# Kernel optimization log

Measured on AMD Instinct MI355X. Metric: run time of the kernel, lower is better.

The kernel has to match this reference:

```python
import jax, jax.numpy as jnp
import numpy as np

NEG = -1e30  # log-space 'minus infinity' that stays finite in fp32 arithmetic
BLANK = 0


def _lse3(a, b, c):
    m = jnp.maximum(jnp.maximum(a, b), c)
    return m + jnp.log(jnp.exp(a - m) + jnp.exp(b - m) + jnp.exp(c - m))


def setup_inputs() -> dict:
    key = jax.random.key(0)
    k1, k2, k3, k4 = jax.random.split(key, 4)
    B, T, C, L = 16, 512, 4096, 128
    scores = jax.random.normal(k1, (B, T, C), dtype=jnp.float32)
    labels = jax.random.randint(k2, (B, L), 1, C, dtype=jnp.int64)      # no blanks in targets
    feat_lens = jax.random.randint(k3, (B,), 384, T + 1, dtype=jnp.int64)
    label_lens = jax.random.randint(k4, (B,), 64, L + 1, dtype=jnp.int64)
    return {"scores": scores, "labels": labels, "feat_lens": feat_lens, "label_lens": label_lens}


def reference(scores, labels, feat_lens, label_lens):
    # scores: [B, T, C]. Matches torch: log_softmax then nn.CTCLoss(blank=0,
    # reduction='mean', zero_infinity=True).
    scores = scores.astype(jnp.float32)
    log_probs = jax.nn.log_softmax(scores, axis=-1)                      # [B, T, C]
    B, T, C = scores.shape
    L = labels.shape[1]
    S = 2 * L + 1  # extended label: blank, l1, blank, ..., lL, blank

    ext = jnp.full((B, S), BLANK, dtype=labels.dtype).at[:, 1::2].set(labels)
    # Gather per-(t, extended-symbol) log-probs once: [B, T, S]
    lp = jnp.take_along_axis(log_probs, jnp.broadcast_to(ext[:, None, :], (B, T, S)), axis=2)

    # skip transition s-2 -> s allowed iff ext[s] != blank and ext[s] != ext[s-2]
    skip = jnp.concatenate(
        [jnp.zeros((B, 2), bool), (ext[:, 2:] != ext[:, :-2]) & (ext[:, 2:] != BLANK)], axis=1)

    alpha0 = jnp.full((B, S), NEG, dtype=jnp.float32).at[:, 0].set(lp[:, 0, 0])
    alpha0 = alpha0.at[:, 1].set(jnp.where(label_lens > 0, lp[:, 0, 1], NEG))

    lp_t_first = jnp.swapaxes(lp, 0, 1)  # [T, B, S]

    def step(alpha, xs):
        lp_t, t = xs
        a1 = jnp.pad(alpha, ((0, 0), (1, 0)), constant_values=NEG)[:, :S]
        a2 = jnp.pad(alpha, ((0, 0), (2, 0)), constant_values=NEG)[:, :S]
        a2 = jnp.where(skip, a2, NEG)
        new = lp_t + _lse3(alpha, a1, a2)
        alpha = jnp.where((t < feat_lens)[:, None], new, alpha)  # freeze past feat_len
        return alpha, None

    alpha, _ = jax.lax.scan(step, alpha0, (lp_t_first[1:], jnp.arange(1, T)))

    end = 2 * label_lens  # index of final blank per sample
    a_end = jnp.take_along_axis(alpha, end[:, None], axis=1)[:, 0]
    a_end1 = jnp.where(
        label_lens > 0,
        jnp.take_along_axis(alpha, jnp.maximum(end - 1, 0)[:, None], axis=1)[:, 0], NEG)
    m = jnp.maximum(a_end, a_end1)
    log_lik = m + jnp.log(jnp.exp(a_end - m) + jnp.exp(a_end1 - m))
    loss = -log_lik
    loss = jnp.where(loss > 0.5e30, 0.0, loss)  # zero_infinity=True
    denom = jnp.maximum(label_lens, 1).astype(loss.dtype)
    return jnp.mean(loss / denom)  # torch 'mean': divide by target_lengths, then batch mean
```

## Files before the change

kernel.cpp:

```cpp
#include <hip/hip_runtime.h>

#define T_ 512
#define C_ 4096
#define L_ 128
#define RCPLN2 1.4426950408889634f
#define LN2 0.6931471805599453f
#define NEGL (-1e30f)
#define SCALE_CTR 4.722366482869645e21f
#define SCALE_LOG 72.0f

__device__ __forceinline__ float fexp2(float x) { return __builtin_amdgcn_exp2f(x); }
__device__ __forceinline__ float flog2(float x) { return __builtin_amdgcn_logf(x); }
__device__ __forceinline__ float frcp(float x)  { return __builtin_amdgcn_rcpf(x); }
__device__ __forceinline__ float lg(float x)    { return (x > 0.f) ? flog2(x) : NEGL; }

template <int CTRL>
__device__ __forceinline__ float dppmov(float v) {
  return __int_as_float(__builtin_amdgcn_update_dpp(
      0, __float_as_int(v), CTRL, 0xF, 0xF, true));
}
__device__ __forceinline__ float wshr1(float v) { return dppmov<0x138>(v); }
__device__ __forceinline__ float wshl1(float v) { return dppmov<0x130>(v); }
template <int CTRL>
__device__ __forceinline__ float maxdpp(float v) {
  return fmaxf(v, dppmov<CTRL>(v));
}
__device__ __forceinline__ float wavemax(float v) {
  v = maxdpp<0xB1>(v);
  v = maxdpp<0x4E>(v);
  v = maxdpp<0x141>(v);
  v = maxdpp<0x140>(v);
  v = maxdpp<0x142>(v);
  v = maxdpp<0x143>(v);
  return __int_as_float(__builtin_amdgcn_readlane(__float_as_int(v), 63));
}

__global__ __launch_bounds__(256) void k_lse_gather(
    const float* __restrict__ scores, const int* __restrict__ labels,
    const int* __restrict__ feat_lens,
    float* __restrict__ p_lab, float* __restrict__ p_blank,
    int* __restrict__ dpDone, float* __restrict__ lossAcc) {
  const int row = blockIdx.x;
  const int b = row >> 9;
  const int t = row & (T_ - 1);
  if (row == 0 && threadIdx.x == 0) {
    atomicExch(dpDone, 0);
    atomicExch(lossAcc, 0.0f);
  }
  if (t >= feat_lens[b]) return;

  __shared__ float sRow[C_];
  __shared__ float sSum[4];
  const float4* __restrict__ rp4 = (const float4*)(scores + (size_t)row * C_);
  float4* sRow4 = (float4*)sRow;
  const int tid = threadIdx.x;

  float s0 = 0.f, s1 = 0.f, s2 = 0.f, s3 = 0.f;
#pragma unroll
  for (int k = 0; k < 4; ++k) {
    float4 v = rp4[tid + 256 * k];
    sRow4[tid + 256 * k] = v;
    s0 += fexp2(v.x * RCPLN2);
    s1 += fexp2(v.y * RCPLN2);
    s2 += fexp2(v.z * RCPLN2);
    s3 += fexp2(v.w * RCPLN2);
  }
  float s = (s0 + s1) + (s2 + s3);
#pragma unroll
  for (int off = 32; off; off >>= 1) s += __shfl_down(s, off);
  const int wid = tid >> 6, lane = tid & 63;
  if (lane == 0) sSum[wid] = s;
  __syncthreads();
  const float l2sum = flog2((sSum[0] + sSum[1]) + (sSum[2] + sSum[3]));

  if (tid < L_) {
    const int lab = labels[b * L_ + tid];
    p_lab[(size_t)row * L_ + tid] = fexp2(sRow[lab] * RCPLN2 - l2sum);
  } else if (tid == L_) {
    p_blank[row] = fexp2(sRow[0] * RCPLN2 - l2sum);
  }
}

__global__ __launch_bounds__(128) void k_ctc_dp(
    const float* __restrict__ p_lab, const float* __restrict__ p_blank,
    const int* __restrict__ labels, const int* __restrict__ feat_lens,
    const int* __restrict__ label_lens, int* __restrict__ dpDone,
    float* __restrict__ lossAcc, float* __restrict__ out, int B) {
  const int b = blockIdx.x;
  const int lane = threadIdx.x & 63;
  const int wid = threadIdx.x >> 6;
  const int flen = feat_lens[b];
  const int llen = label_lens[b];
  const int tm = (flen >> 1) & ~3;

  const int l0 = labels[b * L_ + 2 * lane];
  const int l1 = labels[b * L_ + 2 * lane + 1];
  const int lm1 = __shfl_up(l1, 1);
  const int ln0 = __shfl_down(l0, 1);
  const bool skip1 = (lane > 0) && (l0 != lm1);
  const bool skip3 = (l1 != l0);
  const bool skipd = (lane < 63) && (ln0 != l1);

  const float2* __restrict__ llp = (const float2*)(p_lab + (size_t)b * T_ * L_);
  const float* __restrict__ lpl = p_lab + (size_t)b * T_ * L_;
  const float* __restrict__ lbp = p_blank + b * T_;

  __shared__ float sB[257];
  __shared__ float sSb;

  if (wid == 0) {
    const float2 ll0 = llp[lane];
    float a0 = (lane == 0) ? lbp[0] : 0.f;
    float a1 = (lane == 0) ? ll0.x : 0.f;
    float a2 = 0.f, a3 = 0.f, a4 = 0.f;
    float p = 0.f;
    float Sa = 0.f;

    float2 cc[4], nc[4], mc[4]; float cb[4], nb[4], mb[4];
#pragma unroll
    for (int k = 0; k < 4; ++k) {
      cc[k] = llp[(1 + k) * 64 + lane]; cb[k] = lbp[1 + k];
    }
#pragma unroll
    for (int k = 0; k < 4; ++k) {
      const int tt = min(5 + k, flen - 1);
      nc[k] = llp[tt * 64 + lane]; nb[k] = lbp[tt];
    }
#pragma unroll
    for (int k = 0; k < 4; ++k) {
      const int tt = min(9 + k, flen - 1);
      mc[k] = llp[tt * 64 + lane]; mb[k] = lbp[tt];
    }
    int t = 1;
    while (t <= tm) {
      float2 oc[4]; float ob[4];
#pragma unroll
      for (int k = 0; k < 4; ++k) {
        const int tt = min(t + 12 + k, flen - 1);
        oc[k] = llp[tt * 64 + lane]; ob[k] = lbp[tt];
      }
#pragma unroll
      for (int k = 0; k < 4; ++k) {
        const float n3 = cc[k].y * (a3 + a2 + (skip3 ? a1 : 0.f));
        const float n4 = cb[k] * (a4 + a3);
        const float pn = wshr1(n3);
        const float n0 = cb[k] * (a0 + p);
        const float n1 = cc[k].x * (a1 + a0 + (skip1 ? p : 0.f));
        const float n2 = cb[k] * (a2 + a1);
        a0 = n0; a1 = n1; a2 = n2; a3 = n3;
        a4 = (lane == 63) ? n4 : 0.f;
        p = pn;
        if (k & 1) {
          float m = wavemax(fmaxf(fmaxf(fmaxf(a0, a1), fmaxf(a2, a3)), a4));
          m = fmaxf(m, 1e-35f);
          const float r = frcp(m) * SCALE_CTR;
          Sa += flog2(m) - SCALE_LOG;
          a0 *= r; a1 *= r; a2 *= r; a3 *= r; a4 *= r; p *= r;
        }
      }
#pragma unroll
      for (int k = 0; k < 4; ++k) { cc[k] = nc[k]; cb[k] = nb[k];
                                    nc[k] = mc[k]; nb[k] = mb[k];
                                    mc[k] = oc[k]; mb[k] = ob[k]; }
      t += 4;
    }
    const float2 cce = llp[tm * 64 + lane];
    const float cbe = lbp[tm];
    const float lb2 = flog2(cbe), lc0 = flog2(cce.x), lc1 = flog2(cce.y);
    const float la0 = lg(a0), la1 = lg(a1), la2 = lg(a2), la3 = lg(a3);
    const float la4 = lg(a4);
    __syncthreads();
    float w0 = la0 + sB[4 * lane + 0] - lb2;
    float w1 = la1 + sB[4 * lane + 1] - lc0;
    float w2 = la2 + sB[4 * lane + 2] - lb2;
    float w3 = la3 + sB[4 * lane + 3] - lc1;
    float m = fmaxf(fmaxf(w0, w1), fmaxf(w2, w3));
    float w4 = NEGL;
    if (lane == 63) { w4 = la4 + sB[256] - lb2; m = fmaxf(m, w4); }
#pragma unroll
    for (int off = 1; off < 64; off <<= 1) m = fmaxf(m, __shfl_xor(m, off));
    float sum = fexp2(w0 - m) + fexp2(w1 - m) + fexp2(w2 - m) + fexp2(w3 - m);
    if (lane == 63) sum += fexp2(w4 - m);
#pragma unroll
    for (int off = 1; off < 64; off <<= 1) sum += __shfl_xor(sum, off);
    if (lane == 0) {
      const float l2lik = m + flog2(sum) + Sa + sSb;
      float loss = -LN2 * l2lik;
      if (!(fabsf(loss) < 0.5e30f)) loss = 0.0f;
      atomicAdd(lossAcc, loss / (float)llen);
      const int done = __hip_atomic_fetch_add(dpDone, 1, __ATOMIC_ACQ_REL,
                                              __HIP_MEMORY_SCOPE_AGENT);
      if (done == B - 1)
        out[0] = atomicAdd(lossAcc, 0.0f) / (float)B;
    }
  } else {
    const int e = 2 * llen;
    const float ve = lbp[flen - 1];
    const float vo = lpl[(size_t)(flen - 1) * L_ + (llen - 1)];
    float b0 = (4 * lane == e) ? ve : 0.f;
    float b1 = (4 * lane + 1 == e - 1) ? vo : 0.f;
    float b2 = (4 * lane + 2 == e) ? ve : 0.f;
    float b3 = (4 * lane + 3 == e - 1) ? vo : 0.f;
    float b4 = (lane == 63 && e == 256) ? ve : 0.f;
    float q0 = __shfl_down(b0, 1); q0 = (lane == 63) ? b4 : q0;
    float q1 = __shfl_down(b1, 1); q1 = (lane == 63) ? 0.f : q1;
    float Sb = 0.f;

    float2 cc[4], nc[4], mc[4]; float cb[4], nb[4], mb[4];
    int t = flen - 2;
#pragma unroll
    for (int k = 0; k < 4; ++k) {
      const int tt = max(t - k, tm);
      cc[k] = llp[tt * 64 + lane]; cb[k] = lbp[tt];
    }
#pragma unroll
    for (int k = 0; k < 4; ++k) {
      const int tt = max(t - 4 - k, tm);
      nc[k] = llp[tt * 64 + lane]; nb[k] = lbp[tt];
    }
#pragma unroll
    for (int k = 0; k < 4; ++k) {
      const int tt = max(t - 8 - k, tm);
      mc[k] = llp[tt * 64 + lane]; mb[k] = lbp[tt];
    }
    while (t >= tm) {
      float2 oc[4]; float ob[4];
#pragma unroll
      for (int k = 0; k < 4; ++k) {
        const int tt = max(t - 12 - k, tm);
        oc[k] = llp[tt * 64 + lane]; ob[k] = lbp[tt];
      }
#pragma unroll
      for (int k = 0; k < 4; ++k) {
        if (t - k >= tm) {
          const float n0 = cb[k] * (b0 + b1);
          const float n1 = cc[k].x * (b1 + b2 + (skip3 ? b3 : 0.f));
          const float n4 = cb[k] * b4;
          const float q0n = wshl1(n0);
          const float q1n = wshl1(n1);
          const float n3 = cc[k].y * (b3 + q0 + (skipd ? q1 : 0.f));
          const float n2 = cb[k] * (b2 + b3);
          b0 = n0; b1 = n1; b2 = n2; b3 = n3; b4 = n4;
          q0 = (lane == 63) ? n4 : q0n;
          q1 = q1n;
        }
        if (k & 1) {
          float m = wavemax(fmaxf(fmaxf(fmaxf(b0, b1), fmaxf(b2, b3)), b4));
          m = fmaxf(m, 1e-35f);
          const float r = frcp(m) * SCALE_CTR;
          Sb += flog2(m) - SCALE_LOG;
          b0 *= r; b1 *= r; b2 *= r; b3 *= r; b4 *= r; q0 *= r; q1 *= r;
        }
      }
#pragma unroll
      for (int k = 0; k < 4; ++k) { cc[k] = nc[k]; cb[k] = nb[k];
                                    nc[k] = mc[k]; nb[k] = mb[k];
                                    mc[k] = oc[k]; mb[k] = ob[k]; }
      t -= 4;
    }
    sB[4 * lane + 0] = lg(b0);
    sB[4 * lane + 1] = lg(b1);
    sB[4 * lane + 2] = lg(b2);
    sB[4 * lane + 3] = lg(b3);
    if (lane == 63) sB[256] = lg(b4);
    if (lane == 0) sSb = Sb;
    __syncthreads();
  }
}

extern "C" void kernel_launch(void* const* d_in, const int* in_sizes, int n_in,
                              void* d_out, int out_size, void* d_ws, size_t ws_size,
                              hipStream_t stream) {
  const float* scores = (const float*)d_in[0];
  const int* labels = (const int*)d_in[1];
  const int* feat_lens = (const int*)d_in[2];
  const int* label_lens = (const int*)d_in[3];
  const int B = in_sizes[2];

  int* dpDone = (int*)d_ws;
  float* lossAcc = (float*)d_ws + 1;
  float* p_lab = (float*)d_ws + 64;
  float* p_blank = p_lab + (size_t)B * T_ * L_;
  float* out = (float*)d_out;

  k_lse_gather<<<B * T_, 256, 0, stream>>>(scores, labels, feat_lens,
                                           p_lab, p_blank, dpDone, lossAcc);
  k_ctc_dp<<<B, 128, 0, stream>>>(p_lab, p_blank, labels, feat_lens, label_lens,
                                  dpDone, lossAcc, out, B);
}
```

Before: 221.7 us.

## Stage forward/backward CTC probabilities through shared memory in 32-step chunks

Replaces the per-wave register prefetch pipeline of global loads with a cooperative staging scheme. Each 32-timestep chunk of label and blank probabilities for both the forward and backward passes is loaded into shared memory by all 128 threads using float4 loads, followed by a barrier. Each wave then runs its recurrence reading from LDS. This takes global-load latency off the serial DP chain, but adds two block barriers per chunk and couples the forward and backward waves, so neither can run ahead of the other.

```diff
diff --git a/kernel.cpp b/kernel.cpp
--- a/kernel.cpp
+++ b/kernel.cpp
@@ -87,8 +87,9 @@
     const int* __restrict__ label_lens, int* __restrict__ dpDone,
     float* __restrict__ lossAcc, float* __restrict__ out, int B) {
   const int b = blockIdx.x;
-  const int lane = threadIdx.x & 63;
-  const int wid = threadIdx.x >> 6;
+  const int tid = threadIdx.x;
+  const int lane = tid & 63;
+  const int wid = tid >> 6;
   const int flen = feat_lens[b];
   const int llen = label_lens[b];
   const int tm = (flen >> 1) & ~3;
@@ -105,65 +106,126 @@
   const float* __restrict__ lpl = p_lab + (size_t)b * T_ * L_;
   const float* __restrict__ lbp = p_blank + b * T_;
 
+  __shared__ float sF[32][132];
+  __shared__ float sG[32][132];
   __shared__ float sB[257];
   __shared__ float sSb;
 
+  float a0 = 0.f, a1 = 0.f, a2 = 0.f, a3 = 0.f, a4 = 0.f, pp = 0.f, Sa = 0.f;
+  float b0 = 0.f, b1 = 0.f, b2 = 0.f, b3 = 0.f, b4 = 0.f, q0 = 0.f, q1 = 0.f,
+        Sb = 0.f;
   if (wid == 0) {
     const float2 ll0 = llp[lane];
-    float a0 = (lane == 0) ? lbp[0] : 0.f;
-    float a1 = (lane == 0) ? ll0.x : 0.f;
-    float a2 = 0.f, a3 = 0.f, a4 = 0.f;
-    float p = 0.f;
-    float Sa = 0.f;
-
-    float2 cc[4], nc[4], mc[4]; float cb[4], nb[4], mb[4];
-#pragma unroll
-    for (int k = 0; k < 4; ++k) {
-      cc[k] = llp[(1 + k) * 64 + lane]; cb[k] = lbp[1 + k];
+    a0 = (lane == 0) ? lbp[0] : 0.f;
+    a1 = (lane == 0) ? ll0.x : 0.f;
+  } else {
+    const int e = 2 * llen;
+    const float ve = lbp[flen - 1];
+    const float vo = lpl[(size_t)(flen - 1) * L_ + (llen - 1)];
+    b0 = (4 * lane == e) ? ve : 0.f;
+    b1 = (4 * lane + 1 == e - 1) ? vo : 0.f;
+    b2 = (4 * lane + 2 == e) ? ve : 0.f;
+    b3 = (4 * lane + 3 == e - 1) ? vo : 0.f;
+    b4 = (lane == 63 && e == 256) ? ve : 0.f;
+    q0 = __shfl_down(b0, 1); q0 = (lane == 63) ? b4 : q0;
+    q1 = __shfl_down(b1, 1); q1 = (lane == 63) ? 0.f : q1;
+  }
+
+  int tf = 1;
+  int tb = flen - 2;
+  const int nb = flen - 1 - tm;
+  const int NS = ((tm > nb ? tm : nb) + 31) >> 5;
+
+  for (int ss = 0; ss < NS; ++ss) {
+    const int t0f = 1 + (ss << 5);
+    const int t0b = flen - 2 - (ss << 5);
+    {
+      const int rg = tid >> 5;
+      const int c4 = (tid & 31) << 2;
+#pragma unroll
+      for (int r8 = 0; r8 < 8; ++r8) {
+        const int r = (r8 << 2) + rg;
+        const int tF = min(t0f + r, T_ - 1);
+        const int tB = max(t0b - r, 0);
+        const float4 v = *(const float4*)(lpl + (size_t)tF * L_ + c4);
+        const float4 w = *(const float4*)(lpl + (size_t)tB * L_ + c4);
+        *(float4*)&sF[r][c4] = v;
+        *(float4*)&sG[r][c4] = w;
+      }
+      if (tid >= 64) {
+        const int i = tid - 64;
+        if (i < 32) sF[i][128] = lbp[min(t0f + i, T_ - 1)];
+        else        sG[i - 32][128] = lbp[max(t0b - (i - 32), 0)];
+      }
     }
-#pragma unroll
-    for (int k = 0; k < 4; ++k) {
-      const int tt = min(5 + k, flen - 1);
-      nc[k] = llp[tt * 64 + lane]; nb[k] = lbp[tt];
+    __syncthreads();
+    if (wid == 0) {
+      for (int c = 0; c < 8; ++c) {
+        if (tf <= tm) {
+          const int rbase = tf - t0f;
+#pragma unroll
+          for (int k = 0; k < 4; ++k) {
+            const int r = rbase + k;
+            const float2 cck = *(const float2*)&sF[r][2 * lane];
+            const float cbk = sF[r][128];
+            const float n3 = cck.y * (a3 + a2 + (skip3 ? a1 : 0.f));
+            const float n4 = cbk * (a4 + a3);
+            const float pn = wshr1(n3);
+            const float n0 = cbk * (a0 + pp);
+            const float n1 = cck.x * (a1 + a0 + (skip1 ? pp : 0.f));
+            const float n2 = cbk * (a2 + a1);
+            a0 = n0; a1 = n1; a2 = n2; a3 = n3;
+            a4 = (lane == 63) ? n4 : 0.f;
+            pp = pn;
+            if (k & 1) {
+              float m = wavemax(fmaxf(fmaxf(fmaxf(a0, a1), fmaxf(a2, a3)), a4));
+              m = fmaxf(m, 1e-35f);
+              const float r2 = frcp(m) * SCALE_CTR;
+              Sa += flog2(m) - SCALE_LOG;
+              a0 *= r2; a1 *= r2; a2 *= r2; a3 *= r2; a4 *= r2; pp *= r2;
+            }
+          }
+          tf += 4;
+        }
+      }
+    } else {
+      for (int c = 0; c < 8; ++c) {
+        if (tb >= tm) {
+          const int rbase = t0b - tb;
+#pragma unroll
+          for (int k = 0; k < 4; ++k) {
+            if (tb - k >= tm) {
+              const int r = rbase + k;
+              const float2 cck = *(const float2*)&sG[r][2 * lane];
+              const float cbk = sG[r][128];
+              const float n0 = cbk * (b0 + b1);
+              const float n1 = cck.x * (b1 + b2 + (skip3 ? b3 : 0.f));
+              const float n4 = cbk * b4;
+              const float q0n = wshl1(n0);
+              const float q1n = wshl1(n1);
+              const float n3 = cck.y * (b3 + q0 + (skipd ? q1 : 0.f));
+              const float n2 = cbk * (b2 + b3);
+              b0 = n0; b1 = n1; b2 = n2; b3 = n3; b4 = n4;
+              q0 = (lane == 63) ? n4 : q0n;
+              q1 = q1n;
+            }
+            if (k & 1) {
+              float m = wavemax(fmaxf(fmaxf(fmaxf(b0, b1), fmaxf(b2, b3)), b4));
+              m = fmaxf(m, 1e-35f);
+              const float r2 = frcp(m) * SCALE_CTR;
+              Sb += flog2(m) - SCALE_LOG;
+              b0 *= r2; b1 *= r2; b2 *= r2; b3 *= r2; b4 *= r2;
+              q0 *= r2; q1 *= r2;
+            }
+          }
+          tb -= 4;
+        }
+      }
     }
-#pragma unroll
-    for (int k = 0; k < 4; ++k) {
-      const int tt = min(9 + k, flen - 1);
-      mc[k] = llp[tt * 64 + lane]; mb[k] = lbp[tt];
-    }
-    int t = 1;
-    while (t <= tm) {
-      float2 oc[4]; float ob[4];
-#pragma unroll
-      for (int k = 0; k < 4; ++k) {
-        const int tt = min(t + 12 + k, flen - 1);
-        oc[k] = llp[tt * 64 + lane]; ob[k] = lbp[tt];
-      }
-#pragma unroll
-      for (int k = 0; k < 4; ++k) {
-        const float n3 = cc[k].y * (a3 + a2 + (skip3 ? a1 : 0.f));
-        const float n4 = cb[k] * (a4 + a3);
-        const float pn = wshr1(n3);
-        const float n0 = cb[k] * (a0 + p);
-        const float n1 = cc[k].x * (a1 + a0 + (skip1 ? p : 0.f));
-        const float n2 = cb[k] * (a2 + a1);
-        a0 = n0; a1 = n1; a2 = n2; a3 = n3;
-        a4 = (lane == 63) ? n4 : 0.f;
-        p = pn;
-        if (k & 1) {
-          float m = wavemax(fmaxf(fmaxf(fmaxf(a0, a1), fmaxf(a2, a3)), a4));
-          m = fmaxf(m, 1e-35f);
-          const float r = frcp(m) * SCALE_CTR;
-          Sa += flog2(m) - SCALE_LOG;
-          a0 *= r; a1 *= r; a2 *= r; a3 *= r; a4 *= r; p *= r;
-        }
-      }
-#pragma unroll
-      for (int k = 0; k < 4; ++k) { cc[k] = nc[k]; cb[k] = nb[k];
-                                    nc[k] = mc[k]; nb[k] = mb[k];
-                                    mc[k] = oc[k]; mb[k] = ob[k]; }
-      t += 4;
-    }
+    __syncthreads();
+  }
+
+  if (wid == 0) {
     const float2 cce = llp[tm * 64 + lane];
     const float cbe = lbp[tm];
     const float lb2 = flog2(cbe), lc0 = flog2(cce.x), lc1 = flog2(cce.y);
@@ -194,70 +256,6 @@
         out[0] = atomicAdd(lossAcc, 0.0f) / (float)B;
     }
   } else {
-    const int e = 2 * llen;
-    const float ve = lbp[flen - 1];
-    const float vo = lpl[(size_t)(flen - 1) * L_ + (llen - 1)];
-    float b0 = (4 * lane == e) ? ve : 0.f;
-    float b1 = (4 * lane + 1 == e - 1) ? vo : 0.f;
-    float b2 = (4 * lane + 2 == e) ? ve : 0.f;
-    float b3 = (4 * lane + 3 == e - 1) ? vo : 0.f;
-    float b4 = (lane == 63 && e == 256) ? ve : 0.f;
-    float q0 = __shfl_down(b0, 1); q0 = (lane == 63) ? b4 : q0;
-    float q1 = __shfl_down(b1, 1); q1 = (lane == 63) ? 0.f : q1;
-    float Sb = 0.f;
-
-    float2 cc[4], nc[4], mc[4]; float cb[4], nb[4], mb[4];
-    int t = flen - 2;
-#pragma unroll
-    for (int k = 0; k < 4; ++k) {
-      const int tt = max(t - k, tm);
-      cc[k] = llp[tt * 64 + lane]; cb[k] = lbp[tt];
-    }
-#pragma unroll
-    for (int k = 0; k < 4; ++k) {
-      const int tt = max(t - 4 - k, tm);
-      nc[k] = llp[tt * 64 + lane]; nb[k] = lbp[tt];
-    }
-#pragma unroll
-    for (int k = 0; k < 4; ++k) {
-      const int tt = max(t - 8 - k, tm);
-      mc[k] = llp[tt * 64 + lane]; mb[k] = lbp[tt];
-    }
-    while (t >= tm) {
-      float2 oc[4]; float ob[4];
-#pragma unroll
-      for (int k = 0; k < 4; ++k) {
-        const int tt = max(t - 12 - k, tm);
-        oc[k] = llp[tt * 64 + lane]; ob[k] = lbp[tt];
-      }
-#pragma unroll
-      for (int k = 0; k < 4; ++k) {
-        if (t - k >= tm) {
-          const float n0 = cb[k] * (b0 + b1);
-          const float n1 = cc[k].x * (b1 + b2 + (skip3 ? b3 : 0.f));
-          const float n4 = cb[k] * b4;
-          const float q0n = wshl1(n0);
-          const float q1n = wshl1(n1);
-          const float n3 = cc[k].y * (b3 + q0 + (skipd ? q1 : 0.f));
-          const float n2 = cb[k] * (b2 + b3);
-          b0 = n0; b1 = n1; b2 = n2; b3 = n3; b4 = n4;
-          q0 = (lane == 63) ? n4 : q0n;
-          q1 = q1n;
-        }
-        if (k & 1) {
-          float m = wavemax(fmaxf(fmaxf(fmaxf(b0, b1), fmaxf(b2, b3)), b4));
-          m = fmaxf(m, 1e-35f);
-          const float r = frcp(m) * SCALE_CTR;
-          Sb += flog2(m) - SCALE_LOG;
-          b0 *= r; b1 *= r; b2 *= r; b3 *= r; b4 *= r; q0 *= r; q1 *= r;
-        }
-      }
-#pragma unroll
-      for (int k = 0; k < 4; ++k) { cc[k] = nc[k]; cb[k] = nb[k];
-                                    nc[k] = mc[k]; nb[k] = mb[k];
-                                    mc[k] = oc[k]; mb[k] = ob[k]; }
-      t -= 4;
-    }
     sB[4 * lane + 0] = lg(b0);
     sB[4 * lane + 1] = lg(b1);
     sB[4 * lane + 2] = lg(b2);
```

Result: slower. 227.0 us (+2.4%).
